# Performance work log

Measured on AMD Instinct MI355X. Metric: run time of the kernel, lower is better.

## Reference

```python
import jax, jax.numpy as jnp
import numpy as np

B, T, E, A, D, S, N, K = 256, 64, 1024, 32, 1024, 256, 1024, 5
MIN_STD = 0.1


def setup_inputs() -> dict:
    key = jax.random.key(0)
    ks = jax.random.split(key, 16)
    def w(k, shape, scale=0.02):
        return jax.random.normal(k, shape, jnp.float32) * scale
    return dict(
        seq_len=T,
        obs_embed=jax.random.normal(ks[0], (B, T, E), jnp.float32),
        action=jax.random.normal(ks[1], (B, T, A), jnp.float32),
        nonterms=jnp.ones((B, T, 1), jnp.float32),
        init_deter=jax.random.normal(ks[2], (B, D), jnp.float32),
        init_stoch=jax.random.normal(ks[3], (B, S), jnp.float32),
        noise_prior=jax.random.normal(ks[4], (T - 1, B, S), jnp.float32),
        noise_post=jax.random.normal(ks[5], (T - 1, B, S), jnp.float32),
        W_embed=w(ks[6], (S + A, D)), b_embed=jnp.zeros((D,), jnp.float32),
        W_ens=w(ks[7], (K, D, S)), b_ens=jnp.zeros((K, S), jnp.float32),
        W_ih=w(ks[8], (3 * D, D)), W_hh=w(ks[9], (3 * D, D)),
        b_ih=jnp.zeros((3 * D,), jnp.float32), b_hh=jnp.zeros((3 * D,), jnp.float32),
        Wp1=w(ks[10], (D, N)), bp1=jnp.zeros((N,), jnp.float32),
        Wp2=w(ks[11], (N, 2 * S)), bp2=jnp.zeros((2 * S,), jnp.float32),
        Wq1=w(ks[12], (D + E, N)), bq1=jnp.zeros((N,), jnp.float32),
        Wq2=w(ks[13], (N, 2 * S)), bq2=jnp.zeros((2 * S,), jnp.float32),
    )


def _rollout(obs_embed, action, nonterms, init_deter, init_stoch,
             noise_prior, noise_post, W_embed, b_embed, W_ens, b_ens,
             W_ih, W_hh, b_ih, b_hh, Wp1, bp1, Wp2, bp2, Wq1, bq1, Wq2, bq2):
    elu = jax.nn.elu

    def gru(x, h):  # torch.nn.GRUCell math
        gi = x @ W_ih.T + b_ih
        gh = h @ W_hh.T + b_hh
        ir, iz, ig = jnp.split(gi, 3, axis=-1)
        hr, hz, hg = jnp.split(gh, 3, axis=-1)
        r = jax.nn.sigmoid(ir + hr)
        z = jax.nn.sigmoid(iz + hz)
        n = jnp.tanh(ig + r * hg)
        return (1.0 - z) * n + z * h

    def step(carry, xs):
        deter, stoch = carry
        obs_t, act_t, nt, eps_p, eps_q = xs  # nt: [B,1]
        prev_action = act_t * nt
        sa = elu(jnp.concatenate([stoch * nt, prev_action], -1) @ W_embed + b_embed)
        preds = jnp.einsum('bd,kds->kbs', sa, W_ens) + b_ens[:, None, :]  # ensemble heads
        deter_new = gru(sa, deter * nt)
        pm, ps = jnp.split(elu(deter_new @ Wp1 + bp1) @ Wp2 + bp2, 2, -1)
        ps = jax.nn.softplus(ps) + MIN_STD
        prior_stoch = pm + ps * eps_p
        qm, qs = jnp.split(elu(jnp.concatenate([deter_new, obs_t], -1) @ Wq1 + bq1) @ Wq2 + bq2, 2, -1)
        qs = jax.nn.softplus(qs) + MIN_STD
        post_stoch = qm + qs * eps_q
        prior_cat = jnp.concatenate([pm, ps, prior_stoch, deter_new], -1)   # [B, 3S+D]
        post_cat = jnp.concatenate([qm, qs, post_stoch, deter_new], -1)     # [B, 3S+D]
        disag_flat = jnp.transpose(preds, (1, 0, 2)).reshape(preds.shape[1], -1)  # [B, K*S]
        out = jnp.concatenate([prior_cat, post_cat, disag_flat], -1)
        return (deter_new, post_stoch), out

    Tm1 = noise_prior.shape[0]
    xs = (jnp.swapaxes(obs_embed[:, :Tm1], 0, 1),
          jnp.swapaxes(action[:, :Tm1], 0, 1),
          jnp.swapaxes(nonterms[:, :Tm1], 0, 1),
          noise_prior, noise_post)
    _, outs = jax.lax.scan(step, (init_deter, init_stoch), xs)
    return jnp.swapaxes(outs, 0, 1)  # [B, T-1, 2*(3S+D)+K*S]


def reference(seq_len, obs_embed, action, nonterms, init_deter, init_stoch,
              noise_prior, noise_post, W_embed, b_embed, W_ens, b_ens,
              W_ih, W_hh, b_ih, b_hh, Wp1, bp1, Wp2, bp2, Wq1, bq1, Wq2, bq2):
    return _rollout(obs_embed, action, nonterms, init_deter, init_stoch,
                    noise_prior, noise_post, W_embed, b_embed, W_ens, b_ens,
                    W_ih, W_hh, b_ih, b_hh, Wp1, bp1, Wp2, bp2, Wq1, bq1, Wq2, bq2)
```

## Files before the change

kernel.cpp:

```cpp
#include <hip/hip_runtime.h>

typedef float f32x4 __attribute__((ext_vector_type(4)));
typedef __bf16 bf16x8 __attribute__((ext_vector_type(8)));
typedef unsigned short u16;

#define OUTC 4864
#define OUTT ((size_t)63 * OUTC)

__device__ __forceinline__ u16 f2bf(float f) {
    unsigned u = __float_as_uint(f);
    u += 0x7FFFu + ((u >> 16) & 1u);
    return (u16)(u >> 16);
}
__device__ __forceinline__ float bf2f(u16 h) { return __uint_as_float((unsigned)h << 16); }
__device__ __forceinline__ float fexp(float x) { return __expf(x); }
__device__ __forceinline__ float eluf(float x) { return x > 0.f ? x : fexp(x) - 1.f; }
__device__ __forceinline__ float splus(float x) { return x > 15.f ? x : __logf(1.f + fexp(x)); }
__device__ __forceinline__ float sigm(float x) { return 1.f / (1.f + fexp(-x)); }
__device__ __forceinline__ float tanhfast(float x) { return 2.f / (1.f + fexp(-2.f * x)) - 1.f; }
__device__ __forceinline__ int swz(int row, int cb) { return row * 128 + (cb ^ ((row & 7) << 4)); }

template <int NT, class FA, class FE>
__device__ __forceinline__ void gemmN(char* As, FA fa, const u16* __restrict__ Bt,
                                      int ldb, int n0, int nstr, int K, int m0, FE fe) {
    char* Bs = As + 8192;
    const int tid = threadIdx.x;
    const int lane = tid & 63;
    const int w = tid >> 6;
    const int wr = (w >> 1) * 32, wc = (w & 1) * 32;
    f32x4 acc[NT][4];
    f32x4 zf = {0.f, 0.f, 0.f, 0.f};
#pragma unroll
    for (int j = 0; j < NT; j++)
#pragma unroll
        for (int q = 0; q < 4; q++) acc[j][q] = zf;
    const int r0 = tid >> 3;
    const int ke = (tid & 7) * 8;
    const int cb = (tid & 7) * 16;
    uint4 av0 = fa(m0 + r0, ke);
    uint4 av1 = fa(m0 + r0 + 32, ke);
    uint4 bv[NT][2];
#pragma unroll
    for (int j = 0; j < NT; j++) {
        bv[j][0] = *(const uint4*)(Bt + (size_t)(n0 + j * nstr + r0) * ldb + ke);
        bv[j][1] = *(const uint4*)(Bt + (size_t)(n0 + j * nstr + r0 + 32) * ldb + ke);
    }
    for (int k0 = 0; k0 < K; k0 += 64) {
        __syncthreads();
        *(uint4*)(As + swz(r0, cb)) = av0;
        *(uint4*)(As + swz(r0 + 32, cb)) = av1;
#pragma unroll
        for (int j = 0; j < NT; j++) {
            char* B = Bs + j * 8192;
            *(uint4*)(B + swz(r0, cb)) = bv[j][0];
            *(uint4*)(B + swz(r0 + 32, cb)) = bv[j][1];
        }
        __syncthreads();
        if (k0 + 64 < K) {
            int k1 = k0 + 64 + ke;
            av0 = fa(m0 + r0, k1);
            av1 = fa(m0 + r0 + 32, k1);
#pragma unroll
            for (int j = 0; j < NT; j++) {
                bv[j][0] = *(const uint4*)(Bt + (size_t)(n0 + j * nstr + r0) * ldb + k1);
                bv[j][1] = *(const uint4*)(Bt + (size_t)(n0 + j * nstr + r0 + 32) * ldb + k1);
            }
        }
#pragma unroll
        for (int kk = 0; kk < 64; kk += 32) {
            const int fcb = kk * 2 + (lane >> 4) * 16;
            bf16x8 a0 = *(const bf16x8*)(As + swz(wr + (lane & 15), fcb));
            bf16x8 a1 = *(const bf16x8*)(As + swz(wr + 16 + (lane & 15), fcb));
#pragma unroll
            for (int j = 0; j < NT; j++) {
                char* B = Bs + j * 8192;
                bf16x8 b0 = *(const bf16x8*)(B + swz(wc + (lane & 15), fcb));
                bf16x8 b1 = *(const bf16x8*)(B + swz(wc + 16 + (lane & 15), fcb));
                acc[j][0] = __builtin_amdgcn_mfma_f32_16x16x32_bf16(a0, b0, acc[j][0], 0, 0, 0);
                acc[j][1] = __builtin_amdgcn_mfma_f32_16x16x32_bf16(a0, b1, acc[j][1], 0, 0, 0);
                acc[j][2] = __builtin_amdgcn_mfma_f32_16x16x32_bf16(a1, b0, acc[j][2], 0, 0, 0);
                acc[j][3] = __builtin_amdgcn_mfma_f32_16x16x32_bf16(a1, b1, acc[j][3], 0, 0, 0);
            }
        }
    }
    const int er = (lane >> 4) * 4, ec = lane & 15;
#pragma unroll
    for (int q = 0; q < 4; q++) {
        int rr = m0 + wr + (q >> 1) * 16 + er;
        int cc = n0 + wc + (q & 1) * 16 + ec;
#pragma unroll
        for (int r = 0; r < 4; r++) {
            float vals[NT];
#pragma unroll
            for (int j = 0; j < NT; j++) vals[j] = acc[j][q][r];
            fe(rr + r, cc, vals);
        }
    }
}

__global__ void __launch_bounds__(256) k_cast(const float* __restrict__ in,
                                              u16* __restrict__ out, int n) {
    int i = blockIdx.x * 256 + threadIdx.x;
    if (i < n) out[i] = f2bf(in[i]);
}

__global__ void __launch_bounds__(256) k_transpose(const float* __restrict__ in,
                                                   u16* __restrict__ out,
                                                   int R, int C, int Rpad, int total) {
    int i = blockIdx.x * 256 + threadIdx.x;
    if (i >= total) return;
    int r = i % Rpad;
    int bc = i / Rpad;
    int c = bc % C;
    int bb = bc / C;
    out[i] = (r < R) ? f2bf(in[((size_t)bb * R + r) * C + c]) : (u16)0;
}

__global__ void __launch_bounds__(256) k_init(const float* __restrict__ init_deter,
                                              const float* __restrict__ init_stoch,
                                              const float* __restrict__ action,
                                              const float* __restrict__ nonterms,
                                              float* __restrict__ deter,
                                              u16* __restrict__ h_nt,
                                              u16* __restrict__ x_embed) {
    int idx = blockIdx.x * 256 + threadIdx.x;
    int b = idx >> 10, d = idx & 1023;
    float nt0 = nonterms[b * 64];
    float dv = init_deter[idx];
    deter[idx] = dv;
    h_nt[idx] = f2bf(dv * nt0);
    if (d < 256) {
        x_embed[b * 320 + d] = f2bf(init_stoch[b * 256 + d] * nt0);
    } else if (d < 320) {
        int c = d - 256;
        x_embed[b * 320 + d] = (c < 32) ? f2bf(action[(size_t)b * 2048 + c] * nt0) : (u16)0;
    }
}

__global__ void __launch_bounds__(256) k_obsc(const float* __restrict__ obs,
                                              const u16* __restrict__ Wq1o_t,
                                              u16* __restrict__ OBSC) {
    __shared__ char sm[40960];
    int jid = blockIdx.x;
    int rb = jid >> 2, cg = jid & 3;
    int m0 = rb * 64, n0 = cg * 256;
    auto fa = [&](int r, int k) {
        int tt = r >> 8, bb = r & 255;
        const float* p = obs + ((size_t)bb * 64 + tt) * 1024 + k;
        float4 f0 = *(const float4*)p, f1 = *(const float4*)(p + 4);
        union { u16 h[8]; uint4 q; } x;
        x.h[0] = f2bf(f0.x); x.h[1] = f2bf(f0.y); x.h[2] = f2bf(f0.z); x.h[3] = f2bf(f0.w);
        x.h[4] = f2bf(f1.x); x.h[5] = f2bf(f1.y); x.h[6] = f2bf(f1.z); x.h[7] = f2bf(f1.w);
        return x.q;
    };
    auto fe = [&](int r, int n, const float* v) {
#pragma unroll
        for (int j = 0; j < 4; j++) OBSC[(size_t)r * 1024 + n + j * 64] = f2bf(v[j]);
    };
    gemmN<4>(sm, fa, Wq1o_t, 1024, n0, 64, 1024, m0, fe);
}

__global__ void __launch_bounds__(256) k_sa(const u16* __restrict__ xe,
                                            const u16* __restrict__ Wt,
                                            const float* __restrict__ bias,
                                            u16* __restrict__ sa) {
    __shared__ char sm[16384];
    int m0 = blockIdx.y * 64, n0 = blockIdx.x * 64;
    auto fa = [&](int r, int k) { return *(const uint4*)(xe + r * 320 + k); };
    auto fe = [&](int r, int n, const float* v) {
        sa[r * 1024 + n] = f2bf(eluf(v[0] + bias[n]));
    };
    gemmN<1>(sm, fa, Wt, 320, n0, 0, 320, m0, fe);
}

__global__ void __launch_bounds__(256) k_gemm3072(const u16* __restrict__ A,
                                                  const u16* __restrict__ B,
                                                  const float* __restrict__ bias,
                                                  float* __restrict__ dst) {
    __shared__ char sm[16384];
    int m0 = blockIdx.y * 64, n0 = blockIdx.x * 64;
    auto fa = [&](int r, int k) { return *(const uint4*)(A + r * 1024 + k); };
    auto fe = [&](int r, int n, const float* v) { dst[(size_t)r * 3072 + n] = v[0] + bias[n]; };
    gemmN<1>(sm, fa, B, 1024, n0, 0, 1024, m0, fe);
}

__global__ void __launch_bounds__(256) k_gru(const float* __restrict__ gi,
                                             const float* __restrict__ gh,
                                             float* __restrict__ deter,
                                             const float* __restrict__ nonterms, int t,
                                             u16* __restrict__ deter_hist,
                                             u16* __restrict__ h_nt,
                                             float* __restrict__ out) {
    int idx = blockIdx.x * 256 + threadIdx.x;
    int b = idx >> 10, d = idx & 1023;
    float nt = nonterms[b * 64 + t];
    float h = deter[idx] * nt;
    size_t gb = (size_t)b * 3072;
    float r = sigm(gi[gb + d] + gh[gb + d]);
    float z = sigm(gi[gb + 1024 + d] + gh[gb + 1024 + d]);
    float n = tanhfast(gi[gb + 2048 + d] + r * gh[gb + 2048 + d]);
    float dn = (1.f - z) * n + z * h;
    deter[idx] = dn;
    u16 db = f2bf(dn);
    deter_hist[(size_t)t * 262144 + idx] = db;
    h_nt[idx] = f2bf(dn * nonterms[b * 64 + t + 1]);
    float* ob = out + (size_t)b * OUTT + (size_t)t * OUTC;
    ob[768 + d] = dn;
    ob[2560 + d] = dn;
}

__global__ void __launch_bounds__(256) k_step4(const u16* __restrict__ h_nt,
                                               const u16* __restrict__ Whh_b,
                                               const float* __restrict__ b_hh,
                                               float* __restrict__ gh,
                                               const u16* __restrict__ deter_hist,
                                               const u16* __restrict__ Wq1d_t,
                                               const float* __restrict__ bq1,
                                               const u16* __restrict__ OBSC,
                                               u16* __restrict__ HQ, int t) {
    __shared__ char sm[16384];
    int bid = blockIdx.x;
    if (bid < 192) {
        if (t >= 62) return;
        int m0 = (bid / 48) * 64, n0 = (bid % 48) * 64;
        auto fa = [&](int r, int k) { return *(const uint4*)(h_nt + r * 1024 + k); };
        auto fe = [&](int r, int n, const float* v) { gh[(size_t)r * 3072 + n] = v[0] + b_hh[n]; };
        gemmN<1>(sm, fa, Whh_b, 1024, n0, 0, 1024, m0, fe);
    } else {
        int j = bid - 192;
        int m0 = (j / 16) * 64, n0 = (j % 16) * 64;
        const u16* A = deter_hist + (size_t)t * 262144;
        const u16* ob = OBSC + (size_t)t * 262144;
        auto fa = [&](int r, int k) { return *(const uint4*)(A + r * 1024 + k); };
        auto fe = [&](int r, int n, const float* v) {
            HQ[r * 1024 + n] = f2bf(eluf(v[0] + bq1[n] + bf2f(ob[r * 1024 + n])));
        };
        gemmN<1>(sm, fa, Wq1d_t, 1024, n0, 0, 1024, m0, fe);
    }
}

__global__ void __launch_bounds__(256) k_q2dist(const u16* __restrict__ HQ,
                                                const u16* __restrict__ Wq2_t,
                                                const float* __restrict__ bq2,
                                                const float* __restrict__ noise_q,
                                                const float* __restrict__ nonterms,
                                                const float* __restrict__ action,
                                                float* __restrict__ out,
                                                u16* __restrict__ x_embed, int t) {
    __shared__ char sm[24576];
    int bid = blockIdx.x;
    if (bid < 16) {
        int m0 = (bid >> 2) * 64, n0 = (bid & 3) * 64;
        auto fa = [&](int r, int k) { return *(const uint4*)(HQ + r * 1024 + k); };
        auto fe = [&](int r, int s, const float* v) {
            float m = v[0] + bq2[s];
            float sd = splus(v[1] + bq2[s + 256]) + 0.1f;
            float eps = noise_q[(size_t)t * 65536 + r * 256 + s];
            float st = m + sd * eps;
            float* obp = out + (size_t)r * OUTT + (size_t)t * OUTC + 1792;
            obp[s] = m;
            obp[256 + s] = sd;
            obp[512 + s] = st;
            float ntn = nonterms[r * 64 + t + 1];
            x_embed[r * 320 + s] = f2bf(st * ntn);
        };
        gemmN<2>(sm, fa, Wq2_t, 1024, n0, 256, 1024, m0, fe);
    } else {
        for (int i = (bid - 16) * 256 + threadIdx.x; i < 16384; i += 1024) {
            int b = i >> 6, c = i & 63;
            float ntn = nonterms[b * 64 + t + 1];
            u16 v = 0;
            if (c < 32) v = f2bf(action[(size_t)b * 2048 + (size_t)(t + 1) * 32 + c] * ntn);
            x_embed[b * 320 + 256 + c] = v;
        }
    }
}

__global__ void __launch_bounds__(256) k_ens(const u16* __restrict__ sa_hist,
                                             const u16* __restrict__ Wens_t,
                                             const float* __restrict__ b_ens,
                                             float* __restrict__ out) {
    __shared__ char sm[40960];
    int m0 = blockIdx.y * 64, n0 = blockIdx.x * 256;
    auto fa = [&](int r, int k) { return *(const uint4*)(sa_hist + (size_t)r * 1024 + k); };
    auto fe = [&](int r, int cc, const float* v) {
        int tt = r >> 8, b = r & 255;
        float* op = out + (size_t)b * OUTT + (size_t)tt * OUTC + 3584;
#pragma unroll
        for (int j = 0; j < 4; j++) {
            int n = cc + j * 64;
            op[n] = v[j] + b_ens[n];
        }
    };
    gemmN<4>(sm, fa, Wens_t, 1024, n0, 64, 1024, m0, fe);
}

__global__ void __launch_bounds__(256) k_hp(const u16* __restrict__ deter_hist,
                                            const u16* __restrict__ Wp1_t,
                                            const float* __restrict__ bp1,
                                            u16* __restrict__ HP) {
    __shared__ char sm[40960];
    int m0 = blockIdx.y * 64, n0 = blockIdx.x * 256;
    auto fa = [&](int r, int k) { return *(const uint4*)(deter_hist + (size_t)r * 1024 + k); };
    auto fe = [&](int r, int cc, const float* v) {
#pragma unroll
        for (int j = 0; j < 4; j++) {
            int n = cc + j * 64;
            HP[(size_t)r * 1024 + n] = f2bf(eluf(v[j] + bp1[n]));
        }
    };
    gemmN<4>(sm, fa, Wp1_t, 1024, n0, 64, 1024, m0, fe);
}

__global__ void __launch_bounds__(256) k_p2(const u16* __restrict__ HP,
                                            const u16* __restrict__ Wp2_t,
                                            const float* __restrict__ bp2,
                                            const float* __restrict__ noise_p,
                                            float* __restrict__ out) {
    __shared__ char sm[24576];
    int m0 = blockIdx.y * 64, n0 = blockIdx.x * 64;
    auto fa = [&](int r, int k) { return *(const uint4*)(HP + (size_t)r * 1024 + k); };
    auto fe = [&](int r, int s, const float* v) {
        int tt = r >> 8, b = r & 255;
        float m = v[0] + bp2[s];
        float sd = splus(v[1] + bp2[s + 256]) + 0.1f;
        float eps = noise_p[(size_t)tt * 65536 + b * 256 + s];
        float st = m + sd * eps;
        float* obp = out + (size_t)b * OUTT + (size_t)tt * OUTC;
        obp[s] = m;
        obp[256 + s] = sd;
        obp[512 + s] = st;
    };
    gemmN<2>(sm, fa, Wp2_t, 1024, n0, 256, 1024, m0, fe);
}

extern "C" void kernel_launch(void* const* d_in, const int* in_sizes, int n_in,
                              void* d_out, int out_size, void* d_ws, size_t ws_size,
                              hipStream_t stream) {
    const float* obs = (const float*)d_in[1];
    const float* action = (const float*)d_in[2];
    const float* nonterms = (const float*)d_in[3];
    const float* init_deter = (const float*)d_in[4];
    const float* init_stoch = (const float*)d_in[5];
    const float* noise_p = (const float*)d_in[6];
    const float* noise_q = (const float*)d_in[7];
    const float* W_embed = (const float*)d_in[8];
    const float* b_embed = (const float*)d_in[9];
    const float* W_ens = (const float*)d_in[10];
    const float* b_ens = (const float*)d_in[11];
    const float* W_ih = (const float*)d_in[12];
    const float* W_hh = (const float*)d_in[13];
    const float* b_ih = (const float*)d_in[14];
    const float* b_hh = (const float*)d_in[15];
    const float* Wp1 = (const float*)d_in[16];
    const float* bp1 = (const float*)d_in[17];
    const float* Wp2 = (const float*)d_in[18];
    const float* bp2 = (const float*)d_in[19];
    const float* Wq1 = (const float*)d_in[20];
    const float* bq1 = (const float*)d_in[21];
    const float* Wq2 = (const float*)d_in[22];
    const float* bq2 = (const float*)d_in[23];
    float* out = (float*)d_out;

    char* ws = (char*)d_ws;
    size_t off = 0;
    auto alloc = [&](size_t bytes) {
        void* p = ws + off;
        off += (bytes + 255) & ~(size_t)255;
        return p;
    };
    u16* Wembed_t = (u16*)alloc((size_t)1024 * 320 * 2);
    u16* Wih_b = (u16*)alloc((size_t)3072 * 1024 * 2);
    u16* Whh_b = (u16*)alloc((size_t)3072 * 1024 * 2);
    u16* Wens_t = (u16*)alloc((size_t)1280 * 1024 * 2);
    u16* Wp1_t = (u16*)alloc((size_t)1024 * 1024 * 2);
    u16* Wp2_t = (u16*)alloc((size_t)512 * 1024 * 2);
    u16* Wq1d_t = (u16*)alloc((size_t)1024 * 1024 * 2);
    u16* Wq1o_t = (u16*)alloc((size_t)1024 * 1024 * 2);
    u16* Wq2_t = (u16*)alloc((size_t)512 * 1024 * 2);
    u16* OBSC = (u16*)alloc((size_t)16128 * 1024 * 2);
    u16* sa_hist = (u16*)alloc((size_t)16128 * 1024 * 2);
    u16* deter_hist = (u16*)alloc((size_t)16128 * 1024 * 2);
    u16* x_embed = (u16*)alloc((size_t)256 * 320 * 2);
    u16* h_nt = (u16*)alloc((size_t)256 * 1024 * 2);
    u16* HQ = (u16*)alloc((size_t)256 * 1024 * 2);
    float* deter = (float*)alloc((size_t)256 * 1024 * 4);
    float* gi = (float*)alloc((size_t)256 * 3072 * 4);
    float* gh = (float*)alloc((size_t)256 * 3072 * 4);
    (void)ws_size; (void)in_sizes; (void)n_in; (void)out_size;

    {
        int tot = 1024 * 320;
        k_transpose<<<(tot + 255) / 256, 256, 0, stream>>>(W_embed, Wembed_t, 288, 1024, 320, tot);
        int nc = 3072 * 1024;
        k_cast<<<(nc + 255) / 256, 256, 0, stream>>>(W_ih, Wih_b, nc);
        k_cast<<<(nc + 255) / 256, 256, 0, stream>>>(W_hh, Whh_b, nc);
        tot = 5 * 256 * 1024;
        k_transpose<<<(tot + 255) / 256, 256, 0, stream>>>(W_ens, Wens_t, 1024, 256, 1024, tot);
        tot = 1024 * 1024;
        k_transpose<<<(tot + 255) / 256, 256, 0, stream>>>(Wp1, Wp1_t, 1024, 1024, 1024, tot);
        tot = 512 * 1024;
        k_transpose<<<(tot + 255) / 256, 256, 0, stream>>>(Wp2, Wp2_t, 1024, 512, 1024, tot);
        tot = 1024 * 1024;
        k_transpose<<<(tot + 255) / 256, 256, 0, stream>>>(Wq1, Wq1d_t, 1024, 1024, 1024, tot);
        k_transpose<<<(tot + 255) / 256, 256, 0, stream>>>(Wq1 + 1024 * 1024, Wq1o_t, 1024, 1024, 1024, tot);
        tot = 512 * 1024;
        k_transpose<<<(tot + 255) / 256, 256, 0, stream>>>(Wq2, Wq2_t, 1024, 512, 1024, tot);
    }
    k_init<<<1024, 256, 0, stream>>>(init_deter, init_stoch, action, nonterms,
                                     deter, h_nt, x_embed);
    k_obsc<<<1008, 256, 0, stream>>>(obs, Wq1o_t, OBSC);
    k_gemm3072<<<dim3(48, 4), 256, 0, stream>>>(h_nt, Whh_b, b_hh, gh);

    for (int t = 0; t < 63; t++) {
        u16* sa_t = sa_hist + (size_t)t * 262144;
        k_sa<<<dim3(16, 4), 256, 0, stream>>>(x_embed, Wembed_t, b_embed, sa_t);
        k_gemm3072<<<dim3(48, 4), 256, 0, stream>>>(sa_t, Wih_b, b_ih, gi);
        k_gru<<<1024, 256, 0, stream>>>(gi, gh, deter, nonterms, t, deter_hist, h_nt, out);
        k_step4<<<256, 256, 0, stream>>>(h_nt, Whh_b, b_hh, gh, deter_hist, Wq1d_t,
                                         bq1, OBSC, HQ, t);
        k_q2dist<<<20, 256, 0, stream>>>(HQ, Wq2_t, bq2, noise_q, nonterms, action,
                                         out, x_embed, t);
    }

    k_ens<<<dim3(5, 252), 256, 0, stream>>>(sa_hist, Wens_t, b_ens, out);
    u16* HP = OBSC;
    k_hp<<<dim3(4, 252), 256, 0, stream>>>(deter_hist, Wp1_t, bp1, HP);
    k_p2<<<dim3(4, 252), 256, 0, stream>>>(HP, Wp2_t, bp2, noise_p, out);
}
```

Baseline: 5.471 ms.

## Move ensemble, prior and obs projections into per-step fused kernels

Removes the upfront obs projection and the post-loop batched ensemble and prior-head GEMMs, and computes them inside each recurrent step. The ensemble, W_ih and W_hh GEMMs are merged into one 3D-grid launch, and p1/q1 are merged into another. This drops the large history buffers and the obs-precompute traffic. The trade-off is that large, well-utilised batched GEMMs become small per-step ones on the serial critical path. Precise expf/tanhf also replace the fast exp intrinsics.

```diff
diff --git a/kernel.cpp b/kernel.cpp
--- a/kernel.cpp
+++ b/kernel.cpp
@@ -4,6 +4,9 @@
 typedef __bf16 bf16x8 __attribute__((ext_vector_type(8)));
 typedef unsigned short u16;
 
+#define NB 256
+#define TT 64
+#define AD 32
 #define OUTC 4864
 #define OUTT ((size_t)63 * OUTC)
 
@@ -12,12 +15,9 @@
     u += 0x7FFFu + ((u >> 16) & 1u);
     return (u16)(u >> 16);
 }
-__device__ __forceinline__ float bf2f(u16 h) { return __uint_as_float((unsigned)h << 16); }
-__device__ __forceinline__ float fexp(float x) { return __expf(x); }
-__device__ __forceinline__ float eluf(float x) { return x > 0.f ? x : fexp(x) - 1.f; }
-__device__ __forceinline__ float splus(float x) { return x > 15.f ? x : __logf(1.f + fexp(x)); }
-__device__ __forceinline__ float sigm(float x) { return 1.f / (1.f + fexp(-x)); }
-__device__ __forceinline__ float tanhfast(float x) { return 2.f / (1.f + fexp(-2.f * x)) - 1.f; }
+__device__ __forceinline__ float sigm(float x) { return 1.f / (1.f + expf(-x)); }
+__device__ __forceinline__ float splus(float x) { return x > 15.f ? x : log1pf(expf(x)); }
+__device__ __forceinline__ float eluf(float x) { return x > 0.f ? x : (expf(x) - 1.f); }
 __device__ __forceinline__ int swz(int row, int cb) { return row * 128 + (cb ^ ((row & 7) << 4)); }
 
 template <int NT, class FA, class FE>
@@ -116,16 +116,16 @@
     out[i] = (r < R) ? f2bf(in[((size_t)bb * R + r) * C + c]) : (u16)0;
 }
 
-__global__ void __launch_bounds__(256) k_init(const float* __restrict__ init_deter,
-                                              const float* __restrict__ init_stoch,
-                                              const float* __restrict__ action,
-                                              const float* __restrict__ nonterms,
-                                              float* __restrict__ deter,
-                                              u16* __restrict__ h_nt,
-                                              u16* __restrict__ x_embed) {
+__global__ void __launch_bounds__(256) k_prep0(const float* __restrict__ init_deter,
+                                               const float* __restrict__ init_stoch,
+                                               const float* __restrict__ action,
+                                               const float* __restrict__ nonterms,
+                                               float* __restrict__ deter,
+                                               u16* __restrict__ h_nt,
+                                               u16* __restrict__ x_embed) {
     int idx = blockIdx.x * 256 + threadIdx.x;
     int b = idx >> 10, d = idx & 1023;
-    float nt0 = nonterms[b * 64];
+    float nt0 = nonterms[b * TT + 0];
     float dv = init_deter[idx];
     deter[idx] = dv;
     h_nt[idx] = f2bf(dv * nt0);
@@ -133,37 +133,38 @@
         x_embed[b * 320 + d] = f2bf(init_stoch[b * 256 + d] * nt0);
     } else if (d < 320) {
         int c = d - 256;
-        x_embed[b * 320 + d] = (c < 32) ? f2bf(action[(size_t)b * 2048 + c] * nt0) : (u16)0;
-    }
-}
-
-__global__ void __launch_bounds__(256) k_obsc(const float* __restrict__ obs,
-                                              const u16* __restrict__ Wq1o_t,
-                                              u16* __restrict__ OBSC) {
-    __shared__ char sm[40960];
-    int jid = blockIdx.x;
-    int rb = jid >> 2, cg = jid & 3;
-    int m0 = rb * 64, n0 = cg * 256;
-    auto fa = [&](int r, int k) {
-        int tt = r >> 8, bb = r & 255;
-        const float* p = obs + ((size_t)bb * 64 + tt) * 1024 + k;
-        float4 f0 = *(const float4*)p, f1 = *(const float4*)(p + 4);
-        union { u16 h[8]; uint4 q; } x;
-        x.h[0] = f2bf(f0.x); x.h[1] = f2bf(f0.y); x.h[2] = f2bf(f0.z); x.h[3] = f2bf(f0.w);
-        x.h[4] = f2bf(f1.x); x.h[5] = f2bf(f1.y); x.h[6] = f2bf(f1.z); x.h[7] = f2bf(f1.w);
-        return x.q;
-    };
-    auto fe = [&](int r, int n, const float* v) {
-#pragma unroll
-        for (int j = 0; j < 4; j++) OBSC[(size_t)r * 1024 + n + j * 64] = f2bf(v[j]);
-    };
-    gemmN<4>(sm, fa, Wq1o_t, 1024, n0, 64, 1024, m0, fe);
-}
-
-__global__ void __launch_bounds__(256) k_sa(const u16* __restrict__ xe,
-                                            const u16* __restrict__ Wt,
-                                            const float* __restrict__ bias,
-                                            u16* __restrict__ sa) {
+        x_embed[b * 320 + d] = (c < AD) ? f2bf(action[(size_t)b * TT * AD + c] * nt0) : (u16)0;
+    }
+}
+
+__global__ void __launch_bounds__(256) k_gru(const float* __restrict__ gi,
+                                             const float* __restrict__ gh,
+                                             float* __restrict__ deter,
+                                             const float* __restrict__ nonterms, int t,
+                                             u16* __restrict__ deter_b,
+                                             u16* __restrict__ h_nt,
+                                             float* __restrict__ out) {
+    int idx = blockIdx.x * 256 + threadIdx.x;
+    int b = idx >> 10, d = idx & 1023;
+    float nt = nonterms[b * TT + t];
+    float h = deter[idx] * nt;
+    size_t gb = (size_t)b * 3072;
+    float r = sigm(gi[gb + d] + gh[gb + d]);
+    float z = sigm(gi[gb + 1024 + d] + gh[gb + 1024 + d]);
+    float n = tanhf(gi[gb + 2048 + d] + r * gh[gb + 2048 + d]);
+    float dn = (1.f - z) * n + z * h;
+    deter[idx] = dn;
+    deter_b[idx] = f2bf(dn);
+    h_nt[idx] = f2bf(dn * nonterms[b * TT + t + 1]);
+    float* ob = out + (size_t)b * OUTT + (size_t)t * OUTC;
+    ob[768 + d] = dn;
+    ob[2560 + d] = dn;
+}
+
+__global__ void __launch_bounds__(256) k_gemm_sa(const u16* __restrict__ xe,
+                                                 const u16* __restrict__ Wt,
+                                                 const float* __restrict__ bias,
+                                                 u16* __restrict__ sa) {
     __shared__ char sm[16384];
     int m0 = blockIdx.y * 64, n0 = blockIdx.x * 64;
     auto fa = [&](int r, int k) { return *(const uint4*)(xe + r * 320 + k); };
@@ -173,165 +174,118 @@
     gemmN<1>(sm, fa, Wt, 320, n0, 0, 320, m0, fe);
 }
 
-__global__ void __launch_bounds__(256) k_gemm3072(const u16* __restrict__ A,
-                                                  const u16* __restrict__ B,
-                                                  const float* __restrict__ bias,
-                                                  float* __restrict__ dst) {
+__global__ void __launch_bounds__(256) k_gemm_big(const u16* __restrict__ sa,
+                                                  const u16* __restrict__ hnt,
+                                                  const u16* __restrict__ Wih,
+                                                  const u16* __restrict__ Whh,
+                                                  const u16* __restrict__ Wens,
+                                                  const float* __restrict__ bih,
+                                                  const float* __restrict__ bhh,
+                                                  const float* __restrict__ bens,
+                                                  float* __restrict__ gi,
+                                                  float* __restrict__ gh,
+                                                  float* __restrict__ dout, int t) {
     __shared__ char sm[16384];
+    int z = blockIdx.z;
     int m0 = blockIdx.y * 64, n0 = blockIdx.x * 64;
-    auto fa = [&](int r, int k) { return *(const uint4*)(A + r * 1024 + k); };
-    auto fe = [&](int r, int n, const float* v) { dst[(size_t)r * 3072 + n] = v[0] + bias[n]; };
-    gemmN<1>(sm, fa, B, 1024, n0, 0, 1024, m0, fe);
-}
-
-__global__ void __launch_bounds__(256) k_gru(const float* __restrict__ gi,
-                                             const float* __restrict__ gh,
-                                             float* __restrict__ deter,
-                                             const float* __restrict__ nonterms, int t,
-                                             u16* __restrict__ deter_hist,
-                                             u16* __restrict__ h_nt,
-                                             float* __restrict__ out) {
-    int idx = blockIdx.x * 256 + threadIdx.x;
-    int b = idx >> 10, d = idx & 1023;
-    float nt = nonterms[b * 64 + t];
-    float h = deter[idx] * nt;
-    size_t gb = (size_t)b * 3072;
-    float r = sigm(gi[gb + d] + gh[gb + d]);
-    float z = sigm(gi[gb + 1024 + d] + gh[gb + 1024 + d]);
-    float n = tanhfast(gi[gb + 2048 + d] + r * gh[gb + 2048 + d]);
-    float dn = (1.f - z) * n + z * h;
-    deter[idx] = dn;
-    u16 db = f2bf(dn);
-    deter_hist[(size_t)t * 262144 + idx] = db;
-    h_nt[idx] = f2bf(dn * nonterms[b * 64 + t + 1]);
-    float* ob = out + (size_t)b * OUTT + (size_t)t * OUTC;
-    ob[768 + d] = dn;
-    ob[2560 + d] = dn;
-}
-
-__global__ void __launch_bounds__(256) k_step4(const u16* __restrict__ h_nt,
-                                               const u16* __restrict__ Whh_b,
-                                               const float* __restrict__ b_hh,
-                                               float* __restrict__ gh,
-                                               const u16* __restrict__ deter_hist,
-                                               const u16* __restrict__ Wq1d_t,
-                                               const float* __restrict__ bq1,
-                                               const u16* __restrict__ OBSC,
-                                               u16* __restrict__ HQ, int t) {
+    if (z == 2 && n0 >= 1280) return;
+    const u16* Ap = (z == 1) ? hnt : sa;
+    auto fa = [&](int r, int k) { return *(const uint4*)(Ap + r * 1024 + k); };
+    if (z == 0) {
+        auto fe = [&](int r, int n, const float* v) { gi[(size_t)r * 3072 + n] = v[0] + bih[n]; };
+        gemmN<1>(sm, fa, Wih, 1024, n0, 0, 1024, m0, fe);
+    } else if (z == 1) {
+        auto fe = [&](int r, int n, const float* v) { gh[(size_t)r * 3072 + n] = v[0] + bhh[n]; };
+        gemmN<1>(sm, fa, Whh, 1024, n0, 0, 1024, m0, fe);
+    } else {
+        float* op = dout + (size_t)t * OUTC + 3584;
+        auto fe = [&](int r, int n, const float* v) { op[(size_t)r * OUTT + n] = v[0] + bens[n]; };
+        gemmN<1>(sm, fa, Wens, 1024, n0, 0, 1024, m0, fe);
+    }
+}
+
+__global__ void __launch_bounds__(256) k_gemm_hpq(const u16* __restrict__ dtb,
+                                                  const float* __restrict__ obs,
+                                                  const u16* __restrict__ Wp1t,
+                                                  const u16* __restrict__ Wq1t,
+                                                  const float* __restrict__ bp1,
+                                                  const float* __restrict__ bq1,
+                                                  u16* __restrict__ hp,
+                                                  u16* __restrict__ hq, int t) {
     __shared__ char sm[16384];
-    int bid = blockIdx.x;
-    if (bid < 192) {
-        if (t >= 62) return;
-        int m0 = (bid / 48) * 64, n0 = (bid % 48) * 64;
-        auto fa = [&](int r, int k) { return *(const uint4*)(h_nt + r * 1024 + k); };
-        auto fe = [&](int r, int n, const float* v) { gh[(size_t)r * 3072 + n] = v[0] + b_hh[n]; };
-        gemmN<1>(sm, fa, Whh_b, 1024, n0, 0, 1024, m0, fe);
+    int z = blockIdx.z;
+    int m0 = blockIdx.y * 64, n0 = blockIdx.x * 64;
+    if (z == 0) {
+        auto fa = [&](int r, int k) { return *(const uint4*)(dtb + r * 1024 + k); };
+        auto fe = [&](int r, int n, const float* v) {
+            hp[r * 1024 + n] = f2bf(eluf(v[0] + bp1[n]));
+        };
+        gemmN<1>(sm, fa, Wp1t, 1024, n0, 0, 1024, m0, fe);
     } else {
-        int j = bid - 192;
-        int m0 = (j / 16) * 64, n0 = (j % 16) * 64;
-        const u16* A = deter_hist + (size_t)t * 262144;
-        const u16* ob = OBSC + (size_t)t * 262144;
-        auto fa = [&](int r, int k) { return *(const uint4*)(A + r * 1024 + k); };
+        auto fa = [&](int r, int k) {
+            if (k < 1024) return *(const uint4*)(dtb + r * 1024 + k);
+            const float* q = obs + (size_t)r * (TT * 1024) + (size_t)t * 1024 + (k - 1024);
+            float4 f0 = *(const float4*)q, f1 = *(const float4*)(q + 4);
+            union { u16 u[8]; uint4 v; } x;
+            x.u[0] = f2bf(f0.x); x.u[1] = f2bf(f0.y); x.u[2] = f2bf(f0.z); x.u[3] = f2bf(f0.w);
+            x.u[4] = f2bf(f1.x); x.u[5] = f2bf(f1.y); x.u[6] = f2bf(f1.z); x.u[7] = f2bf(f1.w);
+            return x.v;
+        };
         auto fe = [&](int r, int n, const float* v) {
-            HQ[r * 1024 + n] = f2bf(eluf(v[0] + bq1[n] + bf2f(ob[r * 1024 + n])));
+            hq[r * 1024 + n] = f2bf(eluf(v[0] + bq1[n]));
         };
-        gemmN<1>(sm, fa, Wq1d_t, 1024, n0, 0, 1024, m0, fe);
-    }
-}
-
-__global__ void __launch_bounds__(256) k_q2dist(const u16* __restrict__ HQ,
-                                                const u16* __restrict__ Wq2_t,
-                                                const float* __restrict__ bq2,
-                                                const float* __restrict__ noise_q,
-                                                const float* __restrict__ nonterms,
-                                                const float* __restrict__ action,
-                                                float* __restrict__ out,
-                                                u16* __restrict__ x_embed, int t) {
+        gemmN<1>(sm, fa, Wq1t, 2048, n0, 0, 2048, m0, fe);
+    }
+}
+
+__global__ void __launch_bounds__(256) k_pq_dist(const u16* __restrict__ hp,
+                                                 const u16* __restrict__ hq,
+                                                 const u16* __restrict__ Wp2t,
+                                                 const u16* __restrict__ Wq2t,
+                                                 const float* __restrict__ bp2,
+                                                 const float* __restrict__ bq2,
+                                                 const float* __restrict__ noise_p,
+                                                 const float* __restrict__ noise_q,
+                                                 const float* __restrict__ nonterms,
+                                                 const float* __restrict__ action,
+                                                 float* __restrict__ out,
+                                                 u16* __restrict__ x_embed, int t) {
     __shared__ char sm[24576];
     int bid = blockIdx.x;
-    if (bid < 16) {
-        int m0 = (bid >> 2) * 64, n0 = (bid & 3) * 64;
-        auto fa = [&](int r, int k) { return *(const uint4*)(HQ + r * 1024 + k); };
+    if (bid < 32) {
+        bool isq = bid >= 16;
+        int j = bid & 15;
+        int m0 = (j >> 2) * 64, n0 = (j & 3) * 64;
+        const u16* A = isq ? hq : hp;
+        const u16* B = isq ? Wq2t : Wp2t;
+        const float* b2 = isq ? bq2 : bp2;
+        const float* noise = isq ? noise_q : noise_p;
+        int obase = isq ? 1792 : 0;
+        auto fa = [&](int r, int k) { return *(const uint4*)(A + r * 1024 + k); };
         auto fe = [&](int r, int s, const float* v) {
-            float m = v[0] + bq2[s];
-            float sd = splus(v[1] + bq2[s + 256]) + 0.1f;
-            float eps = noise_q[(size_t)t * 65536 + r * 256 + s];
+            float m = v[0] + b2[s];
+            float sd = splus(v[1] + b2[s + 256]) + 0.1f;
+            float eps = noise[(size_t)t * 65536 + r * 256 + s];
             float st = m + sd * eps;
-            float* obp = out + (size_t)r * OUTT + (size_t)t * OUTC + 1792;
+            float* obp = out + (size_t)r * OUTT + (size_t)t * OUTC + obase;
             obp[s] = m;
             obp[256 + s] = sd;
             obp[512 + s] = st;
-            float ntn = nonterms[r * 64 + t + 1];
-            x_embed[r * 320 + s] = f2bf(st * ntn);
+            if (isq) {
+                float ntn = nonterms[r * TT + t + 1];
+                x_embed[r * 320 + s] = f2bf(st * ntn);
+            }
         };
-        gemmN<2>(sm, fa, Wq2_t, 1024, n0, 256, 1024, m0, fe);
+        gemmN<2>(sm, fa, B, 1024, n0, 256, 1024, m0, fe);
     } else {
-        for (int i = (bid - 16) * 256 + threadIdx.x; i < 16384; i += 1024) {
+        for (int i = (bid - 32) * 256 + threadIdx.x; i < 16384; i += 1024) {
             int b = i >> 6, c = i & 63;
-            float ntn = nonterms[b * 64 + t + 1];
+            float ntn = nonterms[b * TT + t + 1];
             u16 v = 0;
-            if (c < 32) v = f2bf(action[(size_t)b * 2048 + (size_t)(t + 1) * 32 + c] * ntn);
+            if (c < AD) v = f2bf(action[(size_t)b * TT * AD + (size_t)(t + 1) * AD + c] * ntn);
             x_embed[b * 320 + 256 + c] = v;
         }
     }
-}
-
-__global__ void __launch_bounds__(256) k_ens(const u16* __restrict__ sa_hist,
-                                             const u16* __restrict__ Wens_t,
-                                             const float* __restrict__ b_ens,
-                                             float* __restrict__ out) {
-    __shared__ char sm[40960];
-    int m0 = blockIdx.y * 64, n0 = blockIdx.x * 256;
-    auto fa = [&](int r, int k) { return *(const uint4*)(sa_hist + (size_t)r * 1024 + k); };
-    auto fe = [&](int r, int cc, const float* v) {
-        int tt = r >> 8, b = r & 255;
-        float* op = out + (size_t)b * OUTT + (size_t)tt * OUTC + 3584;
-#pragma unroll
-        for (int j = 0; j < 4; j++) {
-            int n = cc + j * 64;
-            op[n] = v[j] + b_ens[n];
-        }
-    };
-    gemmN<4>(sm, fa, Wens_t, 1024, n0, 64, 1024, m0, fe);
-}
-
-__global__ void __launch_bounds__(256) k_hp(const u16* __restrict__ deter_hist,
-                                            const u16* __restrict__ Wp1_t,
-                                            const float* __restrict__ bp1,
-                                            u16* __restrict__ HP) {
-    __shared__ char sm[40960];
-    int m0 = blockIdx.y * 64, n0 = blockIdx.x * 256;
-    auto fa = [&](int r, int k) { return *(const uint4*)(deter_hist + (size_t)r * 1024 + k); };
-    auto fe = [&](int r, int cc, const float* v) {
-#pragma unroll
-        for (int j = 0; j < 4; j++) {
-            int n = cc + j * 64;
-            HP[(size_t)r * 1024 + n] = f2bf(eluf(v[j] + bp1[n]));
-        }
-    };
-    gemmN<4>(sm, fa, Wp1_t, 1024, n0, 64, 1024, m0, fe);
-}
-
-__global__ void __launch_bounds__(256) k_p2(const u16* __restrict__ HP,
-                                            const u16* __restrict__ Wp2_t,
-                                            const float* __restrict__ bp2,
-                                            const float* __restrict__ noise_p,
-                                            float* __restrict__ out) {
-    __shared__ char sm[24576];
-    int m0 = blockIdx.y * 64, n0 = blockIdx.x * 64;
-    auto fa = [&](int r, int k) { return *(const uint4*)(HP + (size_t)r * 1024 + k); };
-    auto fe = [&](int r, int s, const float* v) {
-        int tt = r >> 8, b = r & 255;
-        float m = v[0] + bp2[s];
-        float sd = splus(v[1] + bp2[s + 256]) + 0.1f;
-        float eps = noise_p[(size_t)tt * 65536 + b * 256 + s];
-        float st = m + sd * eps;
-        float* obp = out + (size_t)b * OUTT + (size_t)tt * OUTC;
-        obp[s] = m;
-        obp[256 + s] = sd;
-        obp[512 + s] = st;
-    };
-    gemmN<2>(sm, fa, Wp2_t, 1024, n0, 256, 1024, m0, fe);
 }
 
 extern "C" void kernel_launch(void* const* d_in, const int* in_sizes, int n_in,
@@ -375,18 +329,17 @@
     u16* Wens_t = (u16*)alloc((size_t)1280 * 1024 * 2);
     u16* Wp1_t = (u16*)alloc((size_t)1024 * 1024 * 2);
     u16* Wp2_t = (u16*)alloc((size_t)512 * 1024 * 2);
-    u16* Wq1d_t = (u16*)alloc((size_t)1024 * 1024 * 2);
-    u16* Wq1o_t = (u16*)alloc((size_t)1024 * 1024 * 2);
+    u16* Wq1_t = (u16*)alloc((size_t)1024 * 2048 * 2);
     u16* Wq2_t = (u16*)alloc((size_t)512 * 1024 * 2);
-    u16* OBSC = (u16*)alloc((size_t)16128 * 1024 * 2);
-    u16* sa_hist = (u16*)alloc((size_t)16128 * 1024 * 2);
-    u16* deter_hist = (u16*)alloc((size_t)16128 * 1024 * 2);
     u16* x_embed = (u16*)alloc((size_t)256 * 320 * 2);
     u16* h_nt = (u16*)alloc((size_t)256 * 1024 * 2);
-    u16* HQ = (u16*)alloc((size_t)256 * 1024 * 2);
+    u16* sa = (u16*)alloc((size_t)256 * 1024 * 2);
     float* deter = (float*)alloc((size_t)256 * 1024 * 4);
+    u16* deter_b = (u16*)alloc((size_t)256 * 1024 * 2);
     float* gi = (float*)alloc((size_t)256 * 3072 * 4);
     float* gh = (float*)alloc((size_t)256 * 3072 * 4);
+    u16* hp = (u16*)alloc((size_t)256 * 1024 * 2);
+    u16* hq = (u16*)alloc((size_t)256 * 1024 * 2);
     (void)ws_size; (void)in_sizes; (void)n_in; (void)out_size;
 
     {
@@ -401,30 +354,24 @@
         k_transpose<<<(tot + 255) / 256, 256, 0, stream>>>(Wp1, Wp1_t, 1024, 1024, 1024, tot);
         tot = 512 * 1024;
         k_transpose<<<(tot + 255) / 256, 256, 0, stream>>>(Wp2, Wp2_t, 1024, 512, 1024, tot);
-        tot = 1024 * 1024;
-        k_transpose<<<(tot + 255) / 256, 256, 0, stream>>>(Wq1, Wq1d_t, 1024, 1024, 1024, tot);
-        k_transpose<<<(tot + 255) / 256, 256, 0, stream>>>(Wq1 + 1024 * 1024, Wq1o_t, 1024, 1024, 1024, tot);
+        tot = 1024 * 2048;
+        k_transpose<<<(tot + 255) / 256, 256, 0, stream>>>(Wq1, Wq1_t, 2048, 1024, 2048, tot);
         tot = 512 * 1024;
         k_transpose<<<(tot + 255) / 256, 256, 0, stream>>>(Wq2, Wq2_t, 1024, 512, 1024, tot);
     }
-    k_init<<<1024, 256, 0, stream>>>(init_deter, init_stoch, action, nonterms,
-                                     deter, h_nt, x_embed);
-    k_obsc<<<1008, 256, 0, stream>>>(obs, Wq1o_t, OBSC);
-    k_gemm3072<<<dim3(48, 4), 256, 0, stream>>>(h_nt, Whh_b, b_hh, gh);
+
+    k_prep0<<<1024, 256, 0, stream>>>(init_deter, init_stoch, action, nonterms,
+                                      deter, h_nt, x_embed);
 
     for (int t = 0; t < 63; t++) {
-        u16* sa_t = sa_hist + (size_t)t * 262144;
-        k_sa<<<dim3(16, 4), 256, 0, stream>>>(x_embed, Wembed_t, b_embed, sa_t);
-        k_gemm3072<<<dim3(48, 4), 256, 0, stream>>>(sa_t, Wih_b, b_ih, gi);
-        k_gru<<<1024, 256, 0, stream>>>(gi, gh, deter, nonterms, t, deter_hist, h_nt, out);
-        k_step4<<<256, 256, 0, stream>>>(h_nt, Whh_b, b_hh, gh, deter_hist, Wq1d_t,
-                                         bq1, OBSC, HQ, t);
-        k_q2dist<<<20, 256, 0, stream>>>(HQ, Wq2_t, bq2, noise_q, nonterms, action,
-                                         out, x_embed, t);
-    }
-
-    k_ens<<<dim3(5, 252), 256, 0, stream>>>(sa_hist, Wens_t, b_ens, out);
-    u16* HP = OBSC;
-    k_hp<<<dim3(4, 252), 256, 0, stream>>>(deter_hist, Wp1_t, bp1, HP);
-    k_p2<<<dim3(4, 252), 256, 0, stream>>>(HP, Wp2_t, bp2, noise_p, out);
-}
+        k_gemm_sa<<<dim3(16, 4), 256, 0, stream>>>(x_embed, Wembed_t, b_embed, sa);
+        k_gemm_big<<<dim3(48, 4, 3), 256, 0, stream>>>(sa, h_nt, Wih_b, Whh_b, Wens_t,
+                                                       b_ih, b_hh, b_ens, gi, gh, out, t);
+        k_gru<<<1024, 256, 0, stream>>>(gi, gh, deter, nonterms, t, deter_b, h_nt, out);
+        k_gemm_hpq<<<dim3(16, 4, 2), 256, 0, stream>>>(deter_b, obs, Wp1_t, Wq1_t,
+                                                       bp1, bq1, hp, hq, t);
+        k_pq_dist<<<36, 256, 0, stream>>>(hp, hq, Wp2_t, Wq2_t, bp2, bq2,
+                                          noise_p, noise_q, nonterms, action,
+                                          out, x_embed, t);
+    }
+}
```

After: 8.416 ms. 1.54x slower.
